# Performance work log

Measured on AMD Instinct MI355X. Metric: run time of the kernel, lower is better.

## Reference

```python
import jax, jax.numpy as jnp
import numpy as np

EPS_RMS = 1.1920929e-07  # torch F.rms_norm default eps = finfo(float32).eps
N_EMBD = 64
N_QKV = 256


def _silu(t):
    return t * jax.nn.sigmoid(t)


def _rms_norm(t):
    return t * jax.lax.rsqrt(jnp.mean(t * t, axis=-1, keepdims=True) + EPS_RMS)


def _w_norm(w, n):
    target_std = n ** (-0.5)
    return w * (target_std / (jnp.std(w, ddof=1) + 1e-08))


def setup_inputs() -> dict:
    key = jax.random.key(0)
    ks = jax.random.split(key, 7)
    B, T = 8, 8192
    x = jax.random.normal(ks[0], (B, T, N_EMBD), dtype=jnp.float32)
    y = jax.random.normal(ks[1], (B, T, N_QKV), dtype=jnp.float32)
    # CastedLinear init: uniform(-s, s), s = sqrt(3)/sqrt(in_features)
    def lin(k, out_f, in_f):
        s = (3.0 ** 0.5) * in_f ** (-0.5)
        return jax.random.uniform(k, (out_f, in_f), jnp.float32, -s, s)
    w_qkv = lin(ks[2], 3 * N_QKV, N_EMBD)          # [768, 64]
    w_swiglu = lin(ks[3], 2 * N_EMBD, N_QKV)       # [128, 256]
    w_out = lin(ks[4], N_EMBD, N_EMBD)             # [64, 64]
    out_w = lin(ks[5], N_EMBD, N_EMBD)             # self.out weight [64, 64]
    tao = lin(ks[6], 3, 1)                          # [3, 1]
    return {"x": x, "y": y, "w_qkv": w_qkv, "w_swiglu": w_swiglu,
            "w_out": w_out, "out_w": out_w, "tao": tao}


def reference(x, y, w_qkv, w_swiglu, w_out, out_w, tao):
    B = x.shape[0]
    # SwiGLU branch: F.linear(y, w_swiglu) -> [B,T,2*n_embd], chunk
    uv = jnp.einsum('btq,eq->bte', y, w_swiglu)
    u, v = jnp.split(uv, 2, axis=-1)                 # each [B,T,64]
    y_out = x + jnp.einsum('btd,ed->bte', u * _silu(v), w_out)

    # gates
    g = jnp.clip(jnp.abs(tao), 1e-08, 1.0)           # [3,1]
    alpha, beta, gamma = g[0], g[1], g[2]

    # Hebbian outer-product memory: mean_b(u^T v) * n_embd^-0.5, rms-normed
    ao = jnp.einsum('btd,bte->de', u, v) / B * (N_EMBD ** (-0.5))  # [64,64]
    ao = _rms_norm(ao)

    # update w_qkv
    n1 = _silu(w_qkv @ ao)                            # [768,64]
    w_qkv_new = _w_norm(w_qkv + n1 @ out_w.T, N_EMBD) * alpha

    # update w_swiglu: view(64, 512).T @ ao
    n2 = _silu(w_swiglu.reshape(N_EMBD, 2 * N_QKV).T @ ao)  # [512,64]
    n2 = n2 @ out_w.T                                  # [512,64]
    w_swiglu_new = w_swiglu + n2.T.reshape(2 * N_EMBD, N_QKV)
    w_swiglu_new = _w_norm(w_swiglu_new, N_QKV) * beta

    # update w_out
    n3 = _silu(w_out @ ao)                             # [64,64]
    w_out_new = _w_norm(w_out + n3 @ out_w.T, N_QKV) * gamma

    return (y_out, w_qkv_new, w_swiglu_new, w_out_new)
```

## Files before the change

kernel.cpp:

```cpp
#include <hip/hip_runtime.h>
#include <cstdint>

typedef short short8 __attribute__((ext_vector_type(8)));
typedef short short4_t __attribute__((ext_vector_type(4)));
typedef float floatx4 __attribute__((ext_vector_type(4)));

#define MFMA_BF16 __builtin_amdgcn_mfma_f32_16x16x32_bf16

__device__ __forceinline__ short f2bf(float f) {
  union { float f; unsigned u; } a; a.f = f;
  unsigned r = a.u + 0x7FFFu + ((a.u >> 16) & 1u);
  return (short)(r >> 16);
}
__device__ __forceinline__ float bf2f(short s) {
  union { unsigned u; float f; } a;
  a.u = ((unsigned)(unsigned short)s) << 16;
  return a.f;
}
__device__ __forceinline__ float silu_f(float v) {
  return v / (1.0f + __expf(-v));
}

#define QDIM 256
#define DEMB 64
#define TILE_T 32
#define ITERS 4
#define NBLK1 512
#define YSTR 264
#define TSTR 40
#define HSTR 72

#define OFF_QKV 4194304
#define OFF_SW  4243456
#define OFF_WO  4276224

#define AO_COPIES 16
#define WS_SUMS   65536

__global__ __launch_bounds__(256, 2) void k1_main(
    const float* __restrict__ x, const float* __restrict__ y,
    const float* __restrict__ w_sw, const float* __restrict__ w_out,
    float* __restrict__ y_out, float* __restrict__ ao_copies)
{
  __shared__ __align__(16) short Ylds[2][TILE_T * YSTR];
  __shared__ __align__(16) short UVT[128 * TSTR];
  __shared__ __align__(16) short Hlds[TILE_T * HSTR];

  const int tid  = threadIdx.x;
  const int lane = tid & 63;
  const int wave = tid >> 6;
  const int l15  = lane & 15;
  const int quad = lane >> 4;
  const floatx4 fzero = {0.f, 0.f, 0.f, 0.f};
  const int tok0 = blockIdx.x * (TILE_T * ITERS);

  float4 yreg[8];
  {
    const float4* src = (const float4*)(y + (size_t)tok0 * QDIM);
#pragma unroll
    for (int rep = 0; rep < 8; ++rep) yreg[rep] = src[tid + rep * 256];
  }

  short8 b1[2][8];
#pragma unroll
  for (int nt = 0; nt < 2; ++nt) {
    const float* wr = w_sw + (size_t)(wave * 32 + nt * 16 + l15) * QDIM + quad * 8;
#pragma unroll
    for (int kt = 0; kt < 8; ++kt) {
      float4 f0 = *(const float4*)(wr + kt * 32);
      float4 f1 = *(const float4*)(wr + kt * 32 + 4);
      short8 f = { f2bf(f0.x), f2bf(f0.y), f2bf(f0.z), f2bf(f0.w),
                   f2bf(f1.x), f2bf(f1.y), f2bf(f1.z), f2bf(f1.w) };
      b1[nt][kt] = f;
    }
  }
  short8 b2[2];
#pragma unroll
  for (int kt = 0; kt < 2; ++kt) {
    const float* wr = w_out + (size_t)(wave * 16 + l15) * DEMB + kt * 32 + quad * 8;
    float4 f0 = *(const float4*)(wr);
    float4 f1 = *(const float4*)(wr + 4);
    short8 f = { f2bf(f0.x), f2bf(f0.y), f2bf(f0.z), f2bf(f0.w),
                 f2bf(f1.x), f2bf(f1.y), f2bf(f1.z), f2bf(f1.w) };
    b2[kt] = f;
  }

  floatx4 ao_acc[4];
#pragma unroll
  for (int i = 0; i < 4; ++i) ao_acc[i] = fzero;

  {
#pragma unroll
    for (int rep = 0; rep < 8; ++rep) {
      int i = tid + rep * 256;
      int tok = i >> 6;
      int col = (i & 63) * 4;
      float4 f = yreg[rep];
      short4_t p4 = { f2bf(f.x), f2bf(f.y), f2bf(f.z), f2bf(f.w) };
      *(short4_t*)&Ylds[0][tok * YSTR + col] = p4;
    }
  }
  float xreg[8];
  __syncthreads();

  for (int it = 0; it < ITERS; ++it) {
    const int cur = it & 1;

    if (it + 1 < ITERS) {
      const float4* src = (const float4*)(y + (size_t)(tok0 + (it + 1) * TILE_T) * QDIM);
#pragma unroll
      for (int rep = 0; rep < 8; ++rep) yreg[rep] = src[tid + rep * 256];
    }
    if (it > 0) {
      const int tb = tok0 + (it - 1) * TILE_T;
#pragma unroll
      for (int mt = 0; mt < 2; ++mt) {
        floatx4 acc2 = fzero;
#pragma unroll
        for (int kt = 0; kt < 2; ++kt) {
          short8 a2 = *(const short8*)&Hlds[(mt * 16 + l15) * HSTR + kt * 32 + quad * 8];
          acc2 = MFMA_BF16(a2, b2[kt], acc2, 0, 0, 0);
        }
        int e = wave * 16 + l15;
#pragma unroll
        for (int r = 0; r < 4; ++r) {
          size_t idx = (size_t)(tb + mt * 16 + quad * 4 + r) * DEMB + e;
          y_out[idx] = xreg[mt * 4 + r] + acc2[r];
        }
      }
    }
    floatx4 acc[2][2];
#pragma unroll
    for (int a = 0; a < 2; ++a)
#pragma unroll
      for (int b = 0; b < 2; ++b) acc[a][b] = fzero;
#pragma unroll
    for (int kt = 0; kt < 8; ++kt) {
      short8 a0 = *(const short8*)&Ylds[cur][(l15)      * YSTR + kt * 32 + quad * 8];
      short8 a1 = *(const short8*)&Ylds[cur][(16 + l15) * YSTR + kt * 32 + quad * 8];
      acc[0][0] = MFMA_BF16(a0, b1[0][kt], acc[0][0], 0, 0, 0);
      acc[0][1] = MFMA_BF16(a0, b1[1][kt], acc[0][1], 0, 0, 0);
      acc[1][0] = MFMA_BF16(a1, b1[0][kt], acc[1][0], 0, 0, 0);
      acc[1][1] = MFMA_BF16(a1, b1[1][kt], acc[1][1], 0, 0, 0);
    }
#pragma unroll
    for (int mt = 0; mt < 2; ++mt)
#pragma unroll
      for (int nt = 0; nt < 2; ++nt) {
        short4_t p4;
#pragma unroll
        for (int r = 0; r < 4; ++r) p4[r] = f2bf(acc[mt][nt][r]);
        int c  = wave * 32 + nt * 16 + l15;
        int t0 = mt * 16 + quad * 4;
        *(short4_t*)&UVT[c * TSTR + t0] = p4;
      }
    __syncthreads();

    {
      const float* xb = x + (size_t)(tok0 + it * TILE_T) * DEMB + wave * 16 + l15;
#pragma unroll
      for (int mt = 0; mt < 2; ++mt)
#pragma unroll
        for (int r = 0; r < 4; ++r)
          xreg[mt * 4 + r] = xb[(mt * 16 + quad * 4 + r) * DEMB];
    }
    {
      int d  = tid & 63;
      int t0 = (tid >> 6) * 8;
      short8 u8 = *(const short8*)&UVT[d * TSTR + t0];
      short8 v8 = *(const short8*)&UVT[(64 + d) * TSTR + t0];
#pragma unroll
      for (int j = 0; j < 8; ++j) {
        float h = bf2f(u8[j]) * silu_f(bf2f(v8[j]));
        Hlds[(t0 + j) * HSTR + d] = f2bf(h);
      }
    }
    {
      short8 a3 = *(const short8*)&UVT[(wave * 16 + l15) * TSTR + quad * 8];
#pragma unroll
      for (int et = 0; et < 4; ++et) {
        short8 b3 = *(const short8*)&UVT[(64 + et * 16 + l15) * TSTR + quad * 8];
        ao_acc[et] = MFMA_BF16(a3, b3, ao_acc[et], 0, 0, 0);
      }
    }
    if (it + 1 < ITERS) {
#pragma unroll
      for (int rep = 0; rep < 8; ++rep) {
        int i = tid + rep * 256;
        int tok = i >> 6;
        int col = (i & 63) * 4;
        float4 f = yreg[rep];
        short4_t p4 = { f2bf(f.x), f2bf(f.y), f2bf(f.z), f2bf(f.w) };
        *(short4_t*)&Ylds[1 - cur][tok * YSTR + col] = p4;
      }
    }
    __syncthreads();
  }

  {
    const int tb = tok0 + (ITERS - 1) * TILE_T;
#pragma unroll
    for (int mt = 0; mt < 2; ++mt) {
      floatx4 acc2 = fzero;
#pragma unroll
      for (int kt = 0; kt < 2; ++kt) {
        short8 a2 = *(const short8*)&Hlds[(mt * 16 + l15) * HSTR + kt * 32 + quad * 8];
        acc2 = MFMA_BF16(a2, b2[kt], acc2, 0, 0, 0);
      }
      int e = wave * 16 + l15;
#pragma unroll
      for (int r = 0; r < 4; ++r) {
        size_t idx = (size_t)(tb + mt * 16 + quad * 4 + r) * DEMB + e;
        y_out[idx] = xreg[mt * 4 + r] + acc2[r];
      }
    }
  }

  float* dst = ao_copies + (blockIdx.x & (AO_COPIES - 1)) * 4096;
#pragma unroll
  for (int et = 0; et < 4; ++et)
#pragma unroll
    for (int r = 0; r < 4; ++r) {
      int d = wave * 16 + quad * 4 + r;
      int e = et * 16 + l15;
      atomicAdd(&dst[d * 64 + e], ao_acc[et][r]);
    }
}

__global__ __launch_bounds__(256) void k3_fused(
    const float* __restrict__ w_qkv, const float* __restrict__ w_sw,
    const float* __restrict__ w_out, const float* __restrict__ out_w,
    const float* __restrict__ ao_copies, const float* __restrict__ tao,
    float* __restrict__ out, float* __restrict__ sums,
    unsigned* __restrict__ cnt)
{
  __shared__ float aoFT[64 * 65];
  __shared__ float ssPart[256];
  __shared__ float scRow[64];
  __shared__ __align__(16) short Nlds[4][16 * 72];
  const int tid = threadIdx.x;

#pragma unroll
  for (int k = 0; k < 16; ++k) {
    int idx = k * 256 + tid;
    float v = 0.f;
#pragma unroll
    for (int c = 0; c < AO_COPIES; ++c) v += ao_copies[c * 4096 + idx];
    v *= (1.0f / 64.0f);
    int d = idx >> 6, e = idx & 63;
    aoFT[e * 65 + d] = v;
  }
  __syncthreads();
  {
    int d = tid >> 2, q = tid & 3;
    float ssp = 0.f;
#pragma unroll
    for (int e2 = 0; e2 < 16; ++e2) {
      float v = aoFT[(q * 16 + e2) * 65 + d];
      ssp += v * v;
    }
    ssPart[tid] = ssp;
  }
  __syncthreads();
  if (tid < 64) {
    float ss = ssPart[tid * 4] + ssPart[tid * 4 + 1] +
               ssPart[tid * 4 + 2] + ssPart[tid * 4 + 3];
    scRow[tid] = rsqrtf(ss * (1.0f / 64.0f) + 1.1920929e-07f);
  }
  __syncthreads();

  const int lane = tid & 63;
  const int wave = tid >> 6;
  const int l15  = lane & 15;
  const int quad = lane >> 4;
  const int rid  = blockIdx.x * 4 + wave;
  const floatx4 fzero = {0.f, 0.f, 0.f, 0.f};

  short8 bf[2][4];
#pragma unroll
  for (int kt = 0; kt < 2; ++kt)
#pragma unroll
    for (int nt = 0; nt < 4; ++nt) {
      short8 f;
#pragma unroll
      for (int j = 0; j < 8; ++j) {
        int d = kt * 32 + quad * 8 + j;
        f[j] = f2bf(aoFT[(nt * 16 + l15) * 65 + d] * scRow[d]);
      }
      bf[kt][nt] = f;
    }

  short8 af[2];
  if (rid < 48) {
    const float* wr = w_qkv + (size_t)(rid * 16 + l15) * 64;
#pragma unroll
    for (int kt = 0; kt < 2; ++kt) {
      const float* p = wr + kt * 32 + quad * 8;
      short8 f;
#pragma unroll
      for (int j = 0; j < 8; ++j) f[j] = f2bf(p[j]);
      af[kt] = f;
    }
  } else if (rid < 80) {
    int p0 = (rid - 48) * 16;
#pragma unroll
    for (int kt = 0; kt < 2; ++kt) {
      short8 f;
#pragma unroll
      for (int j = 0; j < 8; ++j) {
        int a = kt * 32 + quad * 8 + j;
        f[j] = f2bf(w_sw[a * 512 + p0 + l15]);
      }
      af[kt] = f;
    }
  } else {
    const float* wr = w_out + (size_t)((rid - 80) * 16 + l15) * 64;
#pragma unroll
    for (int kt = 0; kt < 2; ++kt) {
      const float* p = wr + kt * 32 + quad * 8;
      short8 f;
#pragma unroll
      for (int j = 0; j < 8; ++j) f[j] = f2bf(p[j]);
      af[kt] = f;
    }
  }

  floatx4 acc[4];
#pragma unroll
  for (int nt = 0; nt < 4; ++nt) acc[nt] = fzero;
#pragma unroll
  for (int kt = 0; kt < 2; ++kt)
#pragma unroll
    for (int nt = 0; nt < 4; ++nt)
      acc[nt] = MFMA_BF16(af[kt], bf[kt][nt], acc[nt], 0, 0, 0);
#pragma unroll
  for (int nt = 0; nt < 4; ++nt)
#pragma unroll
    for (int r = 0; r < 4; ++r)
      Nlds[wave][(quad * 4 + r) * 72 + nt * 16 + l15] = f2bf(silu_f(acc[nt][r]));
  __syncthreads();

  float s1 = 0.f, s2 = 0.f;
  int matrix;
  float vals[16];

  if (rid < 48 || rid >= 80) {
    matrix = (rid < 48) ? 0 : 2;
    short8 a2[2];
#pragma unroll
    for (int kt = 0; kt < 2; ++kt)
      a2[kt] = *(const short8*)&Nlds[wave][l15 * 72 + kt * 32 + quad * 8];
    short8 b2w[2][4];
#pragma unroll
    for (int nt = 0; nt < 4; ++nt) {
      const float* wr = out_w + (size_t)(nt * 16 + l15) * 64;
#pragma unroll
      for (int kt = 0; kt < 2; ++kt) {
        const float* p = wr + kt * 32 + quad * 8;
        short8 f;
#pragma unroll
        for (int j = 0; j < 8; ++j) f[j] = f2bf(p[j]);
        b2w[kt][nt] = f;
      }
    }
    floatx4 acc2[4];
#pragma unroll
    for (int nt = 0; nt < 4; ++nt) acc2[nt] = fzero;
#pragma unroll
    for (int kt = 0; kt < 2; ++kt)
#pragma unroll
      for (int nt = 0; nt < 4; ++nt)
        acc2[nt] = MFMA_BF16(a2[kt], b2w[kt][nt], acc2[nt], 0, 0, 0);

    const float* Wsrc = (rid < 48) ? w_qkv : w_out;
    int base_row = (rid < 48) ? rid * 16 : (rid - 80) * 16;
#pragma unroll
    for (int nt = 0; nt < 4; ++nt)
#pragma unroll
      for (int r = 0; r < 4; ++r) {
        int row = base_row + quad * 4 + r;
        int col = nt * 16 + l15;
        float val = Wsrc[row * 64 + col] + acc2[nt][r];
        vals[nt * 4 + r] = val;
        s1 += val; s2 += val * val;
      }
  } else {
    matrix = 1;
    int p0 = (rid - 48) * 16;
    short8 b2s[2];
#pragma unroll
    for (int kt = 0; kt < 2; ++kt)
      b2s[kt] = *(const short8*)&Nlds[wave][l15 * 72 + kt * 32 + quad * 8];
    short8 a2w[4][2];
#pragma unroll
    for (int mt = 0; mt < 4; ++mt) {
      const float* wr = out_w + (size_t)(mt * 16 + l15) * 64;
#pragma unroll
      for (int kt = 0; kt < 2; ++kt) {
        const float* p = wr + kt * 32 + quad * 8;
        short8 f;
#pragma unroll
        for (int j = 0; j < 8; ++j) f[j] = f2bf(p[j]);
        a2w[mt][kt] = f;
      }
    }
    floatx4 acc2[4];
#pragma unroll
    for (int mt = 0; mt < 4; ++mt) acc2[mt] = fzero;
#pragma unroll
    for (int mt = 0; mt < 4; ++mt)
#pragma unroll
      for (int kt = 0; kt < 2; ++kt)
        acc2[mt] = MFMA_BF16(a2w[mt][kt], b2s[kt], acc2[mt], 0, 0, 0);
#pragma unroll
    for (int mt = 0; mt < 4; ++mt)
#pragma unroll
      for (int r = 0; r < 4; ++r) {
        int a = mt * 16 + quad * 4 + r;
        float val = w_sw[a * 512 + p0 + l15] + acc2[mt][r];
        vals[mt * 4 + r] = val;
        s1 += val; s2 += val * val;
      }
  }

#pragma unroll
  for (int off = 32; off > 0; off >>= 1) {
    s1 += __shfl_down(s1, off);
    s2 += __shfl_down(s2, off);
  }
  if (lane == 0) {
    atomicAdd(&sums[matrix * 2],     s1);
    atomicAdd(&sums[matrix * 2 + 1], s2);
    __hip_atomic_fetch_add(cnt, 1u, __ATOMIC_RELEASE, __HIP_MEMORY_SCOPE_AGENT);
  }
  while (__hip_atomic_load(cnt, __ATOMIC_ACQUIRE, __HIP_MEMORY_SCOPE_AGENT) < 84u) {
    __builtin_amdgcn_s_sleep(1);
  }

  float ssum = __hip_atomic_load(&sums[matrix * 2],
                                 __ATOMIC_RELAXED, __HIP_MEMORY_SCOPE_AGENT);
  float ssq  = __hip_atomic_load(&sums[matrix * 2 + 1],
                                 __ATOMIC_RELAXED, __HIP_MEMORY_SCOPE_AGENT);
  float N    = (matrix == 0) ? 49152.f : (matrix == 1) ? 32768.f : 4096.f;
  float tstd = (matrix == 0) ? 0.125f : 0.0625f;
  float mean = ssum / N;
  float var  = (ssq - N * mean * mean) / (N - 1.f);
  float sd   = sqrtf(fmaxf(var, 0.f));
  float g    = fminf(fmaxf(fabsf(tao[matrix]), 1e-8f), 1.0f);
  float scale = g * tstd / (sd + 1e-8f);

  if (rid < 48 || rid >= 80) {
    int base_row = (rid < 48) ? rid * 16 : (rid - 80) * 16;
    int off2     = (rid < 48) ? OFF_QKV : OFF_WO;
#pragma unroll
    for (int nt = 0; nt < 4; ++nt)
#pragma unroll
      for (int r = 0; r < 4; ++r) {
        int row = base_row + quad * 4 + r;
        int col = nt * 16 + l15;
        out[off2 + row * 64 + col] = vals[nt * 4 + r] * scale;
      }
  } else {
    int p0 = (rid - 48) * 16;
#pragma unroll
    for (int mt = 0; mt < 4; ++mt)
#pragma unroll
      for (int r = 0; r < 4; ++r) {
        int a = mt * 16 + quad * 4 + r;
        out[OFF_SW + a * 512 + p0 + l15] = vals[mt * 4 + r] * scale;
      }
  }
}

extern "C" void kernel_launch(void* const* d_in, const int* in_sizes, int n_in,
                              void* d_out, int out_size, void* d_ws, size_t ws_size,
                              hipStream_t stream) {
  const float* x     = (const float*)d_in[0];
  const float* y     = (const float*)d_in[1];
  const float* w_qkv = (const float*)d_in[2];
  const float* w_sw  = (const float*)d_in[3];
  const float* w_out = (const float*)d_in[4];
  const float* out_w = (const float*)d_in[5];
  const float* tao   = (const float*)d_in[6];
  float* out = (float*)d_out;
  float* ws  = (float*)d_ws;

  float* ao_copies = ws;
  float* sums      = ws + WS_SUMS;
  unsigned* cnt    = (unsigned*)(ws + WS_SUMS + 7);

  hipMemsetAsync(d_ws, 0, (WS_SUMS + 8) * sizeof(float), stream);
  k1_main<<<dim3(NBLK1), dim3(256), 0, stream>>>(x, y, w_sw, w_out, out, ao_copies);
  k3_fused<<<dim3(21), dim3(256), 0, stream>>>(w_qkv, w_sw, w_out, out_w,
                                               ao_copies, tao, out, sums, cnt);
}
```

Before: 146.4 us.

## Split k1 work across 8 waves per block to cut per-thread registers

Doubles k1_main's block size from 256 to 512 threads and redistributes each wave's MFMA tiles, so every wave handles one 16-column slice of the UV projection, one m-tile of the output projection and two ao tiles. Per-thread register arrays (y prefetch, weight fragments, accumulators, x values) are halved, and launch bounds now request 4 blocks per CU. The aim is more resident waves to hide global memory latency in this bandwidth-bound kernel. In exchange each A-fragment LDS read is shared across fewer MFMAs, and barriers now synchronize twice as many waves.

```diff
diff --git a/kernel.cpp b/kernel.cpp
--- a/kernel.cpp
+++ b/kernel.cpp
@@ -37,7 +37,7 @@
 #define AO_COPIES 16
 #define WS_SUMS   65536
 
-__global__ __launch_bounds__(256, 2) void k1_main(
+__global__ __launch_bounds__(512, 4) void k1_main(
     const float* __restrict__ x, const float* __restrict__ y,
     const float* __restrict__ w_sw, const float* __restrict__ w_out,
     float* __restrict__ y_out, float* __restrict__ ao_copies)
@@ -51,33 +51,36 @@
   const int wave = tid >> 6;
   const int l15  = lane & 15;
   const int quad = lane >> 4;
+  const int mt   = wave & 1;
+  const int eb   = wave >> 1;
+  const int db   = wave >> 1;
+  const int e0   = (wave & 1) * 2;
   const floatx4 fzero = {0.f, 0.f, 0.f, 0.f};
   const int tok0 = blockIdx.x * (TILE_T * ITERS);
 
-  float4 yreg[8];
+  float4 yreg[4];
   {
     const float4* src = (const float4*)(y + (size_t)tok0 * QDIM);
 #pragma unroll
-    for (int rep = 0; rep < 8; ++rep) yreg[rep] = src[tid + rep * 256];
-  }
-
-  short8 b1[2][8];
-#pragma unroll
-  for (int nt = 0; nt < 2; ++nt) {
-    const float* wr = w_sw + (size_t)(wave * 32 + nt * 16 + l15) * QDIM + quad * 8;
+    for (int rep = 0; rep < 4; ++rep) yreg[rep] = src[tid + rep * 512];
+  }
+
+  short8 b1[8];
+  {
+    const float* wr = w_sw + (size_t)(wave * 16 + l15) * QDIM + quad * 8;
 #pragma unroll
     for (int kt = 0; kt < 8; ++kt) {
       float4 f0 = *(const float4*)(wr + kt * 32);
       float4 f1 = *(const float4*)(wr + kt * 32 + 4);
       short8 f = { f2bf(f0.x), f2bf(f0.y), f2bf(f0.z), f2bf(f0.w),
                    f2bf(f1.x), f2bf(f1.y), f2bf(f1.z), f2bf(f1.w) };
-      b1[nt][kt] = f;
+      b1[kt] = f;
     }
   }
   short8 b2[2];
 #pragma unroll
   for (int kt = 0; kt < 2; ++kt) {
-    const float* wr = w_out + (size_t)(wave * 16 + l15) * DEMB + kt * 32 + quad * 8;
+    const float* wr = w_out + (size_t)(eb * 16 + l15) * DEMB + kt * 32 + quad * 8;
     float4 f0 = *(const float4*)(wr);
     float4 f1 = *(const float4*)(wr + 4);
     short8 f = { f2bf(f0.x), f2bf(f0.y), f2bf(f0.z), f2bf(f0.w),
@@ -85,14 +88,13 @@
     b2[kt] = f;
   }
 
-  floatx4 ao_acc[4];
-#pragma unroll
-  for (int i = 0; i < 4; ++i) ao_acc[i] = fzero;
+  floatx4 ao_acc[2];
+  ao_acc[0] = fzero; ao_acc[1] = fzero;
 
   {
 #pragma unroll
-    for (int rep = 0; rep < 8; ++rep) {
-      int i = tid + rep * 256;
+    for (int rep = 0; rep < 4; ++rep) {
+      int i = tid + rep * 512;
       int tok = i >> 6;
       int col = (i & 63) * 4;
       float4 f = yreg[rep];
@@ -100,7 +102,7 @@
       *(short4_t*)&Ylds[0][tok * YSTR + col] = p4;
     }
   }
-  float xreg[8];
+  float xreg[4];
   __syncthreads();
 
   for (int it = 0; it < ITERS; ++it) {
@@ -109,84 +111,72 @@
     if (it + 1 < ITERS) {
       const float4* src = (const float4*)(y + (size_t)(tok0 + (it + 1) * TILE_T) * QDIM);
 #pragma unroll
-      for (int rep = 0; rep < 8; ++rep) yreg[rep] = src[tid + rep * 256];
+      for (int rep = 0; rep < 4; ++rep) yreg[rep] = src[tid + rep * 512];
     }
     if (it > 0) {
       const int tb = tok0 + (it - 1) * TILE_T;
-#pragma unroll
-      for (int mt = 0; mt < 2; ++mt) {
-        floatx4 acc2 = fzero;
-#pragma unroll
-        for (int kt = 0; kt < 2; ++kt) {
-          short8 a2 = *(const short8*)&Hlds[(mt * 16 + l15) * HSTR + kt * 32 + quad * 8];
-          acc2 = MFMA_BF16(a2, b2[kt], acc2, 0, 0, 0);
-        }
-        int e = wave * 16 + l15;
-#pragma unroll
-        for (int r = 0; r < 4; ++r) {
-          size_t idx = (size_t)(tb + mt * 16 + quad * 4 + r) * DEMB + e;
-          y_out[idx] = xreg[mt * 4 + r] + acc2[r];
-        }
-      }
-    }
-    floatx4 acc[2][2];
-#pragma unroll
-    for (int a = 0; a < 2; ++a)
-#pragma unroll
-      for (int b = 0; b < 2; ++b) acc[a][b] = fzero;
+      floatx4 acc2 = fzero;
+#pragma unroll
+      for (int kt = 0; kt < 2; ++kt) {
+        short8 a2 = *(const short8*)&Hlds[(mt * 16 + l15) * HSTR + kt * 32 + quad * 8];
+        acc2 = MFMA_BF16(a2, b2[kt], acc2, 0, 0, 0);
+      }
+      int e = eb * 16 + l15;
+#pragma unroll
+      for (int r = 0; r < 4; ++r) {
+        size_t idx = (size_t)(tb + mt * 16 + quad * 4 + r) * DEMB + e;
+        y_out[idx] = xreg[r] + acc2[r];
+      }
+    }
+    floatx4 acc[2];
+    acc[0] = fzero; acc[1] = fzero;
 #pragma unroll
     for (int kt = 0; kt < 8; ++kt) {
       short8 a0 = *(const short8*)&Ylds[cur][(l15)      * YSTR + kt * 32 + quad * 8];
       short8 a1 = *(const short8*)&Ylds[cur][(16 + l15) * YSTR + kt * 32 + quad * 8];
-      acc[0][0] = MFMA_BF16(a0, b1[0][kt], acc[0][0], 0, 0, 0);
-      acc[0][1] = MFMA_BF16(a0, b1[1][kt], acc[0][1], 0, 0, 0);
-      acc[1][0] = MFMA_BF16(a1, b1[0][kt], acc[1][0], 0, 0, 0);
-      acc[1][1] = MFMA_BF16(a1, b1[1][kt], acc[1][1], 0, 0, 0);
-    }
-#pragma unroll
-    for (int mt = 0; mt < 2; ++mt)
-#pragma unroll
-      for (int nt = 0; nt < 2; ++nt) {
-        short4_t p4;
-#pragma unroll
-        for (int r = 0; r < 4; ++r) p4[r] = f2bf(acc[mt][nt][r]);
-        int c  = wave * 32 + nt * 16 + l15;
-        int t0 = mt * 16 + quad * 4;
-        *(short4_t*)&UVT[c * TSTR + t0] = p4;
-      }
+      acc[0] = MFMA_BF16(a0, b1[kt], acc[0], 0, 0, 0);
+      acc[1] = MFMA_BF16(a1, b1[kt], acc[1], 0, 0, 0);
+    }
+#pragma unroll
+    for (int m2 = 0; m2 < 2; ++m2) {
+      short4_t p4;
+#pragma unroll
+      for (int r = 0; r < 4; ++r) p4[r] = f2bf(acc[m2][r]);
+      int c  = wave * 16 + l15;
+      int t0 = m2 * 16 + quad * 4;
+      *(short4_t*)&UVT[c * TSTR + t0] = p4;
+    }
     __syncthreads();
 
     {
-      const float* xb = x + (size_t)(tok0 + it * TILE_T) * DEMB + wave * 16 + l15;
-#pragma unroll
-      for (int mt = 0; mt < 2; ++mt)
-#pragma unroll
-        for (int r = 0; r < 4; ++r)
-          xreg[mt * 4 + r] = xb[(mt * 16 + quad * 4 + r) * DEMB];
+      const float* xb = x + (size_t)(tok0 + it * TILE_T) * DEMB + eb * 16 + l15;
+#pragma unroll
+      for (int r = 0; r < 4; ++r)
+        xreg[r] = xb[(mt * 16 + quad * 4 + r) * DEMB];
     }
     {
       int d  = tid & 63;
-      int t0 = (tid >> 6) * 8;
-      short8 u8 = *(const short8*)&UVT[d * TSTR + t0];
-      short8 v8 = *(const short8*)&UVT[(64 + d) * TSTR + t0];
-#pragma unroll
-      for (int j = 0; j < 8; ++j) {
-        float h = bf2f(u8[j]) * silu_f(bf2f(v8[j]));
+      int t0 = (tid >> 6) * 4;
+      short4_t u4 = *(const short4_t*)&UVT[d * TSTR + t0];
+      short4_t v4 = *(const short4_t*)&UVT[(64 + d) * TSTR + t0];
+#pragma unroll
+      for (int j = 0; j < 4; ++j) {
+        float h = bf2f(u4[j]) * silu_f(bf2f(v4[j]));
         Hlds[(t0 + j) * HSTR + d] = f2bf(h);
       }
     }
     {
-      short8 a3 = *(const short8*)&UVT[(wave * 16 + l15) * TSTR + quad * 8];
-#pragma unroll
-      for (int et = 0; et < 4; ++et) {
-        short8 b3 = *(const short8*)&UVT[(64 + et * 16 + l15) * TSTR + quad * 8];
-        ao_acc[et] = MFMA_BF16(a3, b3, ao_acc[et], 0, 0, 0);
+      short8 a3 = *(const short8*)&UVT[(db * 16 + l15) * TSTR + quad * 8];
+#pragma unroll
+      for (int i = 0; i < 2; ++i) {
+        short8 b3 = *(const short8*)&UVT[(64 + (e0 + i) * 16 + l15) * TSTR + quad * 8];
+        ao_acc[i] = MFMA_BF16(a3, b3, ao_acc[i], 0, 0, 0);
       }
     }
     if (it + 1 < ITERS) {
 #pragma unroll
-      for (int rep = 0; rep < 8; ++rep) {
-        int i = tid + rep * 256;
+      for (int rep = 0; rep < 4; ++rep) {
+        int i = tid + rep * 512;
         int tok = i >> 6;
         int col = (i & 63) * 4;
         float4 f = yreg[rep];
@@ -199,31 +189,28 @@
 
   {
     const int tb = tok0 + (ITERS - 1) * TILE_T;
-#pragma unroll
-    for (int mt = 0; mt < 2; ++mt) {
-      floatx4 acc2 = fzero;
-#pragma unroll
-      for (int kt = 0; kt < 2; ++kt) {
-        short8 a2 = *(const short8*)&Hlds[(mt * 16 + l15) * HSTR + kt * 32 + quad * 8];
-        acc2 = MFMA_BF16(a2, b2[kt], acc2, 0, 0, 0);
-      }
-      int e = wave * 16 + l15;
-#pragma unroll
-      for (int r = 0; r < 4; ++r) {
-        size_t idx = (size_t)(tb + mt * 16 + quad * 4 + r) * DEMB + e;
-        y_out[idx] = xreg[mt * 4 + r] + acc2[r];
-      }
+    floatx4 acc2 = fzero;
+#pragma unroll
+    for (int kt = 0; kt < 2; ++kt) {
+      short8 a2 = *(const short8*)&Hlds[(mt * 16 + l15) * HSTR + kt * 32 + quad * 8];
+      acc2 = MFMA_BF16(a2, b2[kt], acc2, 0, 0, 0);
+    }
+    int e = eb * 16 + l15;
+#pragma unroll
+    for (int r = 0; r < 4; ++r) {
+      size_t idx = (size_t)(tb + mt * 16 + quad * 4 + r) * DEMB + e;
+      y_out[idx] = xreg[r] + acc2[r];
     }
   }
 
   float* dst = ao_copies + (blockIdx.x & (AO_COPIES - 1)) * 4096;
 #pragma unroll
-  for (int et = 0; et < 4; ++et)
+  for (int i = 0; i < 2; ++i)
 #pragma unroll
     for (int r = 0; r < 4; ++r) {
-      int d = wave * 16 + quad * 4 + r;
-      int e = et * 16 + l15;
-      atomicAdd(&dst[d * 64 + e], ao_acc[et][r]);
+      int d = db * 16 + quad * 4 + r;
+      int e = (e0 + i) * 16 + l15;
+      atomicAdd(&dst[d * 64 + e], ao_acc[i][r]);
     }
 }
 
@@ -490,7 +477,7 @@
   unsigned* cnt    = (unsigned*)(ws + WS_SUMS + 7);
 
   hipMemsetAsync(d_ws, 0, (WS_SUMS + 8) * sizeof(float), stream);
-  k1_main<<<dim3(NBLK1), dim3(256), 0, stream>>>(x, y, w_sw, w_out, out, ao_copies);
+  k1_main<<<dim3(NBLK1), dim3(512), 0, stream>>>(x, y, w_sw, w_out, out, ao_copies);
   k3_fused<<<dim3(21), dim3(256), 0, stream>>>(w_qkv, w_sw, w_out, out_w,
                                                ao_copies, tao, out, sums, cnt);
 }
```

Measured after the change: 144.6 us. No clear change (-1.2%).
